# Kernel optimization log

Hardware: AMD Instinct MI355X
Metric: run time of the kernel (lower is better)

The kernel has to match this reference:

```python
import jax, jax.numpy as jnp
import numpy as np

BS, Q, S1, S2 = 8, 128, 32, 64
H_DIM, NH = 768, 12
DH = H_DIM // NH


def _linear_params(k, scale=0.02):
    kw, _ = jax.random.split(k)
    w = jax.random.normal(kw, (H_DIM, H_DIM), jnp.float32) * scale
    b = jnp.zeros((H_DIM,), jnp.float32)
    return w, b


def setup_inputs() -> dict:
    root = jax.random.key(0)
    ks = jax.random.split(root, 12)
    wq_w, wq_b = _linear_params(ks[0])
    wk_w, wk_b = _linear_params(ks[1])
    wv_w, wv_b = _linear_params(ks[2])
    sq_w, sq_b = _linear_params(ks[3])
    sk_w, sk_b = _linear_params(ks[4])
    sv_w, sv_b = _linear_params(ks[5])
    return {
        "q_in": jax.random.normal(ks[6], (BS, Q, H_DIM), jnp.float32),
        "k_in": jax.random.normal(ks[7], (BS, S1, S2, H_DIM), jnp.float32),
        "v_in": jax.random.normal(ks[8], (BS, S1, S2, H_DIM), jnp.float32),
        "kvec": jax.random.normal(ks[9], (BS, S1, H_DIM), jnp.float32),
        "word_mask": jnp.ones((BS, S1, S2), jnp.int32),
        "sentence_mask": jnp.ones((BS * Q, S1), jnp.int32),
        "wq_w": wq_w, "wq_b": wq_b, "wk_w": wk_w, "wk_b": wk_b,
        "wv_w": wv_w, "wv_b": wv_b, "sq_w": sq_w, "sq_b": sq_b,
        "sk_w": sk_w, "sk_b": sk_b, "sv_w": sv_w, "sv_b": sv_b,
    }


def reference(q_in, k_in, v_in, kvec, word_mask, sentence_mask,
              wq_w, wq_b, wk_w, wk_b, wv_w, wv_b,
              sq_w, sq_b, sk_w, sk_b, sv_w, sv_b):
    bs, q_len = q_in.shape[0], q_in.shape[1]
    s1, s2 = k_in.shape[1], k_in.shape[2]
    scale = 1.0 / jnp.sqrt(jnp.float32(DH))

    # additive masks, as in the torch module
    wm = (1.0 - word_mask.astype(jnp.float32)) * -10000.0      # [bs, s1, s2]
    sm = (1.0 - sentence_mask.astype(jnp.float32)) * -10000.0  # [bs*Q, s1]

    # ---- word-level attention ----
    q = (q_in @ wq_w + wq_b).reshape(bs, q_len, NH, DH)
    k = (k_in @ wk_w + wk_b).reshape(bs, s1, s2, NH, DH)
    v = (v_in @ wv_w + wv_b).reshape(bs, s1, s2, NH, DH)
    # scores over tokens within each sentence: [bs, s1, H, Q, s2]
    scores1 = jnp.einsum('bqhd,bsthd->bshqt', q, k) * scale
    probs1 = jax.nn.softmax(scores1 + wm[:, :, None, None, :], axis=-1)
    # word_hidden: [bs, Q, s1, h]
    wh = jnp.einsum('bshqt,bsthd->bqshd', probs1, v).reshape(bs, q_len, s1, H_DIM)

    # ---- sentence-level attention ----
    sq = (q_in @ sq_w + sq_b).reshape(bs, q_len, NH, DH)
    sk = (kvec @ sk_w + sk_b).reshape(bs, s1, NH, DH)   # shared across queries
    sv = (wh @ sv_w + sv_b).reshape(bs, q_len, s1, NH, DH)
    scores2 = jnp.einsum('bqhd,bshd->bqhs', sq, sk) * scale  # [bs, Q, H, s1]
    scores2 = scores2 + sm.reshape(bs, q_len, s1)[:, :, None, :]
    probs2 = jax.nn.softmax(scores2, axis=-1)
    out = jnp.einsum('bqhs,bqshd->bqhd', probs2, sv).reshape(bs * q_len, H_DIM)
    return out
```

## Files before the change

kernel.cpp:

```cpp
#include <hip/hip_runtime.h>
#include <hip/hip_bf16.h>


typedef __attribute__((ext_vector_type(8))) short short8;
typedef __attribute__((ext_vector_type(4))) short short4v;
typedef __attribute__((ext_vector_type(4))) float f32x4;

__device__ __forceinline__ short f2bf(float f) {
  __hip_bfloat16 b = __float2bfloat16(f);
  return __builtin_bit_cast(short, b);
}
__device__ __forceinline__ float bf2f(short s) {
  __hip_bfloat16 b = __builtin_bit_cast(__hip_bfloat16, s);
  return __bfloat162float(b);
}

#define MFMA16(a, b, c) __builtin_amdgcn_mfma_f32_16x16x32_bf16((a), (b), (c), 0, 0, 0)

__device__ __forceinline__ void async_load16(const short* g, short* l) {
  auto l3 = (__attribute__((address_space(3))) short*)(uintptr_t)(
      reinterpret_cast<uintptr_t>(l));
  auto g1 = (const __attribute__((address_space(1))) short*)g;
  __builtin_amdgcn_global_load_lds((const __attribute__((address_space(1))) void*)g1,
                                   (__attribute__((address_space(3))) void*)l3, 16, 0, 0);
}

__global__ __launch_bounds__(256)
void cvt_all(const float* __restrict__ q_in, const float* __restrict__ k_in,
             const float* __restrict__ v_in, const float* __restrict__ kvec,
             short* __restrict__ qbf, short* __restrict__ kbf,
             short* __restrict__ vbf, short* __restrict__ kvb) {
  const int i = blockIdx.x * 256 + threadIdx.x;
  const float* src;
  short* dst;
  int idx;
  if (i < 98304)        { src = q_in; dst = qbf; idx = i; }
  else if (i < 1671168) { src = k_in; dst = kbf; idx = i - 98304; }
  else if (i < 3244032) { src = v_in; dst = vbf; idx = i - 1671168; }
  else if (i < 3268608) { src = kvec; dst = kvb; idx = i - 3244032; }
  else return;
  const float4* s = (const float4*)src + (size_t)idx * 2;
  const float4 a = s[0], b = s[1];
  __align__(16) short tmp[8] = {f2bf(a.x), f2bf(a.y), f2bf(a.z), f2bf(a.w),
                                f2bf(b.x), f2bf(b.y), f2bf(b.z), f2bf(b.w)};
  *((short8*)dst + idx) = *(short8*)tmp;
}

__global__ __launch_bounds__(256)
void transpose_w6(const float* __restrict__ w0, const float* __restrict__ w1,
                  const float* __restrict__ w2, const float* __restrict__ w3,
                  const float* __restrict__ w4, const float* __restrict__ w5,
                  short* __restrict__ WT) {
  __shared__ float tile[32][33];
  const float* Ws[6] = {w0, w1, w2, w3, w4, w5};
  const float* W = Ws[blockIdx.z];
  short* WTo = WT + (size_t)blockIdx.z * 768 * 768;
  const int bx = blockIdx.x * 32, by = blockIdx.y * 32;
  const int tx = threadIdx.x, ty = threadIdx.y;
  #pragma unroll
  for (int i = 0; i < 32; i += 8)
    tile[ty + i][tx] = W[(size_t)(by + ty + i) * 768 + bx + tx];
  __syncthreads();
  #pragma unroll
  for (int i = 0; i < 32; i += 8)
    WTo[(size_t)(bx + ty + i) * 768 + by + tx] = f2bf(tile[tx][ty + i]);
}

template<int OUT_MODE>
__global__ __launch_bounds__(256)
void gemm_lds(const short* __restrict__ A, const short* __restrict__ WT,
              const float* __restrict__ bias, const float* __restrict__ bias2,
              const float* __restrict__ probs2, void* __restrict__ Outp,
              void* __restrict__ Outp2) {
  const int K = 768;
  __shared__ __align__(16) short As[128 * 32];
  __shared__ __align__(16) short Bs[128 * 32];
  const int tid = threadIdx.x;
  const int m0 = blockIdx.x * 128, n0 = blockIdx.y * 128;
  const int w = tid >> 6, lane = tid & 63, quad = lane >> 4, l16 = lane & 15;
  const int wm = (w >> 1) * 64, wn = (w & 1) * 64;

  const int grow = w * 32 + (lane >> 2);
  const int kc = (lane & 3) * 8;
  const short* ag = A + (size_t)(m0 + grow) * K + kc;
  const short* bg = WT + (size_t)(n0 + grow) * K + kc;
  short* al = &As[(w * 32) * 32];
  short* bl = &Bs[(w * 32) * 32];

  const f32x4 zero4 = {0.f, 0.f, 0.f, 0.f};
  f32x4 acc[4][4];
  #pragma unroll
  for (int i = 0; i < 4; i++)
    #pragma unroll
    for (int j = 0; j < 4; j++) acc[i][j] = zero4;

  for (int k0 = 0; k0 < K; k0 += 32) {
    __syncthreads();
    async_load16(ag, al);
    async_load16(ag + (size_t)16 * K, al + 16 * 32);
    async_load16(bg, bl);
    async_load16(bg + (size_t)16 * K, bl + 16 * 32);
    ag += 32;
    bg += 32;
    __syncthreads();
    short8 af[4], bf[4];
    #pragma unroll
    for (int i = 0; i < 4; i++)
      af[i] = *(short8*)&As[(wm + i * 16 + l16) * 32 + quad * 8];
    #pragma unroll
    for (int j = 0; j < 4; j++)
      bf[j] = *(short8*)&Bs[(wn + j * 16 + l16) * 32 + quad * 8];
    #pragma unroll
    for (int i = 0; i < 4; i++)
      #pragma unroll
      for (int j = 0; j < 4; j++)
        acc[i][j] = MFMA16(af[i], bf[j], acc[i][j]);
  }

  if (OUT_MODE == 4) {
    const int h = (n0 + wn) >> 6;
    const int bq0 = (m0 + wm) >> 5;
    float p2[2][2][4];
    #pragma unroll
    for (int g2 = 0; g2 < 2; g2++)
      #pragma unroll
      for (int par = 0; par < 2; par++)
        #pragma unroll
        for (int r = 0; r < 4; r++)
          p2[g2][par][r] =
              probs2[((size_t)(bq0 + g2) * 12 + h) * 32 + par * 16 + quad * 4 + r];
    float red[4][2];
    #pragma unroll
    for (int j = 0; j < 4; j++)
      #pragma unroll
      for (int g2 = 0; g2 < 2; g2++) {
        float ps = 0.f;
        #pragma unroll
        for (int par = 0; par < 2; par++)
          #pragma unroll
          for (int r = 0; r < 4; r++)
            ps += p2[g2][par][r] * acc[g2 * 2 + par][j][r];
        ps += __shfl_xor(ps, 16);
        ps += __shfl_xor(ps, 32);
        red[j][g2] = ps;
      }
    const int col = n0 + wn + quad * 16 + l16;
    const float bv = bias[col];
    float* outp = (float*)Outp;
    #pragma unroll
    for (int g2 = 0; g2 < 2; g2++)
      outp[(size_t)(bq0 + g2) * 768 + col] = red[quad][g2] + bv;
    return;
  }

  #pragma unroll
  for (int i = 0; i < 4; i++) {
    #pragma unroll
    for (int j = 0; j < 4; j++) {
      const int col = n0 + wn + j * 16 + l16;
      float bv;
      if (OUT_MODE == 3)
        bv = (col < 768) ? bias[col] : bias2[col - 768];
      else
        bv = bias[col];
      #pragma unroll
      for (int r = 0; r < 4; r++) {
        const int g = m0 + wm + i * 16 + quad * 4 + r;
        const float v = acc[i][j][r] + bv;
        if (OUT_MODE == 0) {
          ((float*)Outp)[(size_t)g * 768 + col] = v;
        } else {
          if (col < 768)
            ((short*)Outp)[(size_t)g * 768 + col] = f2bf(v);
          else
            ((float*)Outp2)[(size_t)g * 768 + (col - 768)] = v;
        }
      }
    }
  }
}

__global__ __launch_bounds__(256)
void gemm_kv(const short* __restrict__ kbf, const short* __restrict__ vbf,
             const short* __restrict__ WTk, const short* __restrict__ WTv,
             const float* __restrict__ kbias, const float* __restrict__ vbias,
             short* __restrict__ kp, short* __restrict__ vT) {
  const int K = 768;
  __shared__ __align__(16) short As[128 * 32];
  __shared__ __align__(16) short Bs[128 * 32];
  const int z = blockIdx.z;
  const short* A = z ? vbf : kbf;
  const short* WT = z ? WTv : WTk;
  const float* bias = z ? vbias : kbias;
  const int tid = threadIdx.x;
  const int m0 = blockIdx.x * 128, n0 = blockIdx.y * 128;
  const int w = tid >> 6, lane = tid & 63, quad = lane >> 4, l16 = lane & 15;
  const int wm = (w >> 1) * 64, wn = (w & 1) * 64;

  const int grow = w * 32 + (lane >> 2);
  const int kc = (lane & 3) * 8;
  const short* ag = A + (size_t)(m0 + grow) * K + kc;
  const short* bg = WT + (size_t)(n0 + grow) * K + kc;
  short* al = &As[(w * 32) * 32];
  short* bl = &Bs[(w * 32) * 32];

  const f32x4 zero4 = {0.f, 0.f, 0.f, 0.f};
  f32x4 acc[4][4];
  #pragma unroll
  for (int i = 0; i < 4; i++)
    #pragma unroll
    for (int j = 0; j < 4; j++) acc[i][j] = zero4;

  for (int k0 = 0; k0 < K; k0 += 32) {
    __syncthreads();
    async_load16(ag, al);
    async_load16(ag + (size_t)16 * K, al + 16 * 32);
    async_load16(bg, bl);
    async_load16(bg + (size_t)16 * K, bl + 16 * 32);
    ag += 32;
    bg += 32;
    __syncthreads();
    short8 af[4], bf[4];
    #pragma unroll
    for (int i = 0; i < 4; i++)
      af[i] = *(short8*)&As[(wm + i * 16 + l16) * 32 + quad * 8];
    #pragma unroll
    for (int j = 0; j < 4; j++)
      bf[j] = *(short8*)&Bs[(wn + j * 16 + l16) * 32 + quad * 8];
    #pragma unroll
    for (int i = 0; i < 4; i++)
      #pragma unroll
      for (int j = 0; j < 4; j++)
        acc[i][j] = MFMA16(af[i], bf[j], acc[i][j]);
  }

  if (z == 0) {
    #pragma unroll
    for (int i = 0; i < 4; i++)
      #pragma unroll
      for (int j = 0; j < 4; j++) {
        const int col = n0 + wn + j * 16 + l16;
        const float bv = bias[col];
        #pragma unroll
        for (int r = 0; r < 4; r++) {
          const int g = m0 + wm + i * 16 + quad * 4 + r;
          kp[(size_t)g * 768 + col] = f2bf(acc[i][j][r] + bv);
        }
      }
  } else {
    const int bs_ = (m0 + wm) >> 6;
    const int hh = (n0 + wn) >> 6;
    #pragma unroll
    for (int i = 0; i < 4; i++) {
      const int t0 = i * 16 + quad * 4;
      #pragma unroll
      for (int j = 0; j < 4; j++) {
        const int dd = j * 16 + l16;
        const float bv = bias[hh * 64 + dd];
        __align__(8) short tmp[4];
        #pragma unroll
        for (int r = 0; r < 4; r++) tmp[r] = f2bf(acc[i][j][r] + bv);
        *(short4v*)&vT[(((size_t)bs_ * 12 + hh) * 64 + dd) * 64 + t0] = *(short4v*)tmp;
      }
    }
  }
}

__global__ __launch_bounds__(256)
void word_attn(const short* __restrict__ q_proj, const short* __restrict__ k_proj,
               const short* __restrict__ vT, const int* __restrict__ word_mask,
               short* __restrict__ wh) {
  __shared__ __align__(16) short KVs[128 * 72];
  __shared__ __align__(16) short Ps[128 * 72];
  short* Ks = KVs;
  short* Vs = KVs + 64 * 72;
  short* Os = KVs;

  const int bid = blockIdx.x;
  const int h = bid % 12, s = (bid / 12) % 32, b = bid / (12 * 32);
  const int tid = threadIdx.x;
  const int w = tid >> 6, lane = tid & 63, quad = lane >> 4, l16 = lane & 15;
  const f32x4 zero4 = {0.f, 0.f, 0.f, 0.f};

  {
    const int t2 = tid & 127;
    const int row = t2 >> 1, half = (t2 & 1) * 32;
    const short* src;
    short* dst;
    if (tid < 128) {
      src = k_proj + ((size_t)((b * 32 + s) * 64 + row)) * 768 + h * 64 + half;
      dst = &Ks[row * 72 + half];
    } else {
      src = vT + ((size_t)((b * 32 + s) * 12 + h)) * 4096 + row * 64 + half;
      dst = &Vs[row * 72 + half];
    }
    #pragma unroll
    for (int i = 0; i < 4; i++)
      *(short8*)(dst + i * 8) = *(const short8*)(src + i * 8);
  }
  __syncthreads();

  f32x4 sac[2][4];
  #pragma unroll
  for (int i = 0; i < 2; i++)
    #pragma unroll
    for (int j = 0; j < 4; j++) sac[i][j] = zero4;
  {
    short8 aq[2][2], bk[4][2];
    #pragma unroll
    for (int i = 0; i < 2; i++)
      #pragma unroll
      for (int kb = 0; kb < 2; kb++)
        aq[i][kb] = *(const short8*)(q_proj +
            ((size_t)(b * 128 + w * 32 + i * 16 + l16)) * 768 + h * 64 + kb * 32 + quad * 8);
    #pragma unroll
    for (int j = 0; j < 4; j++)
      #pragma unroll
      for (int kb = 0; kb < 2; kb++)
        bk[j][kb] = *(short8*)&Ks[(j * 16 + l16) * 72 + kb * 32 + quad * 8];
    #pragma unroll
    for (int i = 0; i < 2; i++)
      #pragma unroll
      for (int j = 0; j < 4; j++) {
        sac[i][j] = MFMA16(aq[i][0], bk[j][0], sac[i][j]);
        sac[i][j] = MFMA16(aq[i][1], bk[j][1], sac[i][j]);
      }
  }

  {
    float wmv[4];
    const int* wmp = word_mask + (b * 32 + s) * 64;
    #pragma unroll
    for (int j = 0; j < 4; j++)
      wmv[j] = (1.0f - (float)wmp[j * 16 + l16]) * -10000.0f;
    #pragma unroll
    for (int i = 0; i < 2; i++) {
      #pragma unroll
      for (int r = 0; r < 4; r++) {
        float vv[4];
        float mx = -3.0e38f;
        #pragma unroll
        for (int j = 0; j < 4; j++) {
          const float val = sac[i][j][r] * 0.125f + wmv[j];
          vv[j] = val;
          mx = fmaxf(mx, val);
        }
        mx = fmaxf(mx, __shfl_xor(mx, 1));
        mx = fmaxf(mx, __shfl_xor(mx, 2));
        mx = fmaxf(mx, __shfl_xor(mx, 4));
        mx = fmaxf(mx, __shfl_xor(mx, 8));
        float sum = 0.f;
        #pragma unroll
        for (int j = 0; j < 4; j++) {
          vv[j] = __expf(vv[j] - mx);
          sum += vv[j];
        }
        sum += __shfl_xor(sum, 1);
        sum += __shfl_xor(sum, 2);
        sum += __shfl_xor(sum, 4);
        sum += __shfl_xor(sum, 8);
        const float inv = 1.0f / sum;
        const int row = w * 32 + i * 16 + quad * 4 + r;
        #pragma unroll
        for (int j = 0; j < 4; j++)
          Ps[row * 72 + j * 16 + l16] = f2bf(vv[j] * inv);
      }
    }
  }
  __syncthreads();

  f32x4 oac[2][4];
  #pragma unroll
  for (int i = 0; i < 2; i++)
    #pragma unroll
    for (int j = 0; j < 4; j++) oac[i][j] = zero4;
  {
    short8 ap[2][2], bv[4][2];
    #pragma unroll
    for (int i = 0; i < 2; i++)
      #pragma unroll
      for (int kb = 0; kb < 2; kb++)
        ap[i][kb] = *(short8*)&Ps[(w * 32 + i * 16 + l16) * 72 + kb * 32 + quad * 8];
    #pragma unroll
    for (int j = 0; j < 4; j++)
      #pragma unroll
      for (int kb = 0; kb < 2; kb++)
        bv[j][kb] = *(short8*)&Vs[(j * 16 + l16) * 72 + kb * 32 + quad * 8];
    #pragma unroll
    for (int i = 0; i < 2; i++)
      #pragma unroll
      for (int j = 0; j < 4; j++) {
        oac[i][j] = MFMA16(ap[i][0], bv[j][0], oac[i][j]);
        oac[i][j] = MFMA16(ap[i][1], bv[j][1], oac[i][j]);
      }
  }
  __syncthreads();
  #pragma unroll
  for (int i = 0; i < 2; i++)
    #pragma unroll
    for (int j = 0; j < 4; j++)
      #pragma unroll
      for (int r = 0; r < 4; r++)
        Os[(w * 32 + i * 16 + quad * 4 + r) * 72 + j * 16 + l16] = f2bf(oac[i][j][r]);
  __syncthreads();

  {
    const int row = tid >> 1, half = (tid & 1) * 32;
    short* dst = wh + (((size_t)(b * 128 + row)) * 32 + s) * 768 + h * 64 + half;
    const short* src = &Os[row * 72 + half];
    #pragma unroll
    for (int i = 0; i < 4; i++)
      *(short8*)(dst + i * 8) = *(const short8*)(src + i * 8);
  }
}

__global__ __launch_bounds__(256)
void sent_probs(const float* __restrict__ sq, const float* __restrict__ sk,
                const int* __restrict__ sent_mask, float* __restrict__ probs2) {
  __shared__ float sc[12 * 33];
  const int bid = blockIdx.x;
  const int b = bid >> 7, q = bid & 127;
  const int tid = threadIdx.x;

  for (int p = tid; p < 384; p += 256) {
    const int hh = p >> 5, ss = p & 31;
    const float4* a = (const float4*)(sq + ((size_t)(b * 128 + q)) * 768 + hh * 64);
    const float4* c = (const float4*)(sk + ((size_t)(b * 32 + ss)) * 768 + hh * 64);
    float d = 0.f;
    #pragma unroll
    for (int i = 0; i < 16; i++) {
      const float4 av = a[i], cv = c[i];
      d += av.x * cv.x + av.y * cv.y + av.z * cv.z + av.w * cv.w;
    }
    d = d * 0.125f + (1.0f - (float)sent_mask[(b * 128 + q) * 32 + ss]) * -10000.0f;
    sc[hh * 33 + ss] = d;
  }
  __syncthreads();
  if (tid < 12) {
    float mx = -3.0e38f;
    for (int ss = 0; ss < 32; ss++) mx = fmaxf(mx, sc[tid * 33 + ss]);
    float sum = 0.f;
    for (int ss = 0; ss < 32; ss++) {
      const float e = __expf(sc[tid * 33 + ss] - mx);
      sc[tid * 33 + ss] = e;
      sum += e;
    }
    const float inv = 1.0f / sum;
    for (int ss = 0; ss < 32; ss++) sc[tid * 33 + ss] *= inv;
  }
  __syncthreads();
  for (int p = tid; p < 384; p += 256) {
    const int hh = p >> 5, ss = p & 31;
    probs2[((size_t)bid * 12 + hh) * 32 + ss] = sc[hh * 33 + ss];
  }
}

extern "C" void kernel_launch(void* const* d_in, const int* in_sizes, int n_in,
                              void* d_out, int out_size, void* d_ws, size_t ws_size,
                              hipStream_t stream) {
  (void)in_sizes; (void)n_in; (void)out_size; (void)ws_size;
  const float* q_in      = (const float*)d_in[0];
  const float* k_in      = (const float*)d_in[1];
  const float* v_in      = (const float*)d_in[2];
  const float* kvec      = (const float*)d_in[3];
  const int*   word_mask = (const int*)d_in[4];
  const int*   sent_mask = (const int*)d_in[5];
  const float* wq_w = (const float*)d_in[6],  *wq_b = (const float*)d_in[7];
  const float* wk_w = (const float*)d_in[8],  *wk_b = (const float*)d_in[9];
  const float* wv_w = (const float*)d_in[10], *wv_b = (const float*)d_in[11];
  const float* sq_w = (const float*)d_in[12], *sq_b = (const float*)d_in[13];
  const float* sk_w = (const float*)d_in[14], *sk_b = (const float*)d_in[15];
  const float* sv_w = (const float*)d_in[16], *sv_b = (const float*)d_in[17];
  float* out = (float*)d_out;

  char* ws = (char*)d_ws;
  size_t off = 0;
  auto alloc = [&](size_t bytes) -> void* {
    void* p = ws + off;
    off += (bytes + 255) & ~(size_t)255;
    return p;
  };
  short* WT  = (short*)alloc((size_t)6 * 768 * 768 * 2);
  short* qbf = (short*)alloc((size_t)1024 * 768 * 2);
  short* kbf = (short*)alloc((size_t)16384 * 768 * 2);
  short* vbf = (short*)alloc((size_t)16384 * 768 * 2);
  short* kvb = (short*)alloc((size_t)256 * 768 * 2);
  short* qp  = (short*)alloc((size_t)1024 * 768 * 2);
  short* kp  = (short*)alloc((size_t)16384 * 768 * 2);
  short* vT  = (short*)alloc((size_t)16384 * 768 * 2);
  float* sqp = (float*)alloc((size_t)1024 * 768 * 4);
  float* skp = (float*)alloc((size_t)256 * 768 * 4);
  short* wh  = (short*)alloc((size_t)32768 * 768 * 2);
  float* pr2 = (float*)alloc((size_t)1024 * 12 * 32 * 4);

  const int WELEM = 768 * 768;

  transpose_w6<<<dim3(24, 24, 6), dim3(32, 8), 0, stream>>>(
      wq_w, sq_w, wk_w, wv_w, sk_w, sv_w, WT);
  cvt_all<<<dim3(12768), 256, 0, stream>>>(q_in, k_in, v_in, kvec, qbf, kbf, vbf, kvb);

  gemm_lds<3><<<dim3(8, 12), 256, 0, stream>>>(qbf, WT + 0 * WELEM, wq_b, sq_b,
                                               nullptr, qp, sqp);
  gemm_kv<<<dim3(128, 6, 2), 256, 0, stream>>>(kbf, vbf, WT + 2 * WELEM, WT + 3 * WELEM,
                                               wk_b, wv_b, kp, vT);
  gemm_lds<0><<<dim3(2, 6), 256, 0, stream>>>(kvb, WT + 4 * WELEM, sk_b, nullptr,
                                              nullptr, skp, nullptr);

  word_attn<<<dim3(3072), 256, 0, stream>>>(qp, kp, vT, word_mask, wh);

  sent_probs<<<dim3(1024), 256, 0, stream>>>(sqp, skp, sent_mask, pr2);

  gemm_lds<4><<<dim3(256, 6), 256, 0, stream>>>(wh, WT + 5 * WELEM, sv_b, nullptr,
                                                pr2, out, nullptr);
}
```

Before: 367.7 us.

## Fuse fp32-to-bf16 input conversion into projection GEMM loads with swizzled LDS

Removes the separate cvt_all pass over q/k/v/kvec. The projection GEMMs now load fp32 activations straight into LDS with async global-to-LDS copies and convert to bf16 while reading the MFMA fragments. This avoids writing and re-reading large bf16 copies of k_in and v_in. It also adds XOR swizzles to the A and B LDS layouts to reduce bank conflicts, and merges gemm_kv into a templated gemm. The cost is twice the LDS footprint and global traffic per A tile, plus conversion ALU work inside the inner loop.

```diff
diff --git a/kernel.cpp b/kernel.cpp
--- a/kernel.cpp
+++ b/kernel.cpp
@@ -17,33 +17,11 @@
 
 #define MFMA16(a, b, c) __builtin_amdgcn_mfma_f32_16x16x32_bf16((a), (b), (c), 0, 0, 0)
 
-__device__ __forceinline__ void async_load16(const short* g, short* l) {
-  auto l3 = (__attribute__((address_space(3))) short*)(uintptr_t)(
+__device__ __forceinline__ void async_load16(const void* g, void* l) {
+  auto l3 = (__attribute__((address_space(3))) void*)(uintptr_t)(
       reinterpret_cast<uintptr_t>(l));
-  auto g1 = (const __attribute__((address_space(1))) short*)g;
-  __builtin_amdgcn_global_load_lds((const __attribute__((address_space(1))) void*)g1,
-                                   (__attribute__((address_space(3))) void*)l3, 16, 0, 0);
-}
-
-__global__ __launch_bounds__(256)
-void cvt_all(const float* __restrict__ q_in, const float* __restrict__ k_in,
-             const float* __restrict__ v_in, const float* __restrict__ kvec,
-             short* __restrict__ qbf, short* __restrict__ kbf,
-             short* __restrict__ vbf, short* __restrict__ kvb) {
-  const int i = blockIdx.x * 256 + threadIdx.x;
-  const float* src;
-  short* dst;
-  int idx;
-  if (i < 98304)        { src = q_in; dst = qbf; idx = i; }
-  else if (i < 1671168) { src = k_in; dst = kbf; idx = i - 98304; }
-  else if (i < 3244032) { src = v_in; dst = vbf; idx = i - 1671168; }
-  else if (i < 3268608) { src = kvec; dst = kvb; idx = i - 3244032; }
-  else return;
-  const float4* s = (const float4*)src + (size_t)idx * 2;
-  const float4 a = s[0], b = s[1];
-  __align__(16) short tmp[8] = {f2bf(a.x), f2bf(a.y), f2bf(a.z), f2bf(a.w),
-                                f2bf(b.x), f2bf(b.y), f2bf(b.z), f2bf(b.w)};
-  *((short8*)dst + idx) = *(short8*)tmp;
+  auto g1 = (const __attribute__((address_space(1))) void*)g;
+  __builtin_amdgcn_global_load_lds(g1, l3, 16, 0, 0);
 }
 
 __global__ __launch_bounds__(256)
@@ -66,26 +44,41 @@
     WTo[(size_t)(bx + ty + i) * 768 + by + tx] = f2bf(tile[tx][ty + i]);
 }
 
-template<int OUT_MODE>
+template<int A_FP32, int OUT_MODE>
 __global__ __launch_bounds__(256)
-void gemm_lds(const short* __restrict__ A, const short* __restrict__ WT,
-              const float* __restrict__ bias, const float* __restrict__ bias2,
-              const float* __restrict__ probs2, void* __restrict__ Outp,
-              void* __restrict__ Outp2) {
-  const int K = 768;
-  __shared__ __align__(16) short As[128 * 32];
+void gemm(const void* __restrict__ Ap, const void* __restrict__ Ap2,
+          const short* __restrict__ WTa, const short* __restrict__ WTb,
+          const float* __restrict__ bias_a, const float* __restrict__ bias_b,
+          const float* __restrict__ probs2, void* __restrict__ Outp,
+          void* __restrict__ Outp2) {
+  __shared__ __align__(16) short As[A_FP32 ? 128 * 64 : 128 * 32];
   __shared__ __align__(16) short Bs[128 * 32];
+  float* Alf = (float*)As;
+
+  const int z = (OUT_MODE == 5) ? blockIdx.z : 0;
+  const void* A = (OUT_MODE == 5 && z) ? Ap2 : Ap;
+  const short* WT = (OUT_MODE == 5 && z) ? WTb : WTa;
+  const float* bias = (OUT_MODE == 5 && z) ? bias_b : bias_a;
+
   const int tid = threadIdx.x;
   const int m0 = blockIdx.x * 128, n0 = blockIdx.y * 128;
   const int w = tid >> 6, lane = tid & 63, quad = lane >> 4, l16 = lane & 15;
   const int wm = (w >> 1) * 64, wn = (w & 1) * 64;
 
-  const int grow = w * 32 + (lane >> 2);
-  const int kc = (lane & 3) * 8;
-  const short* ag = A + (size_t)(m0 + grow) * K + kc;
-  const short* bg = WT + (size_t)(n0 + grow) * K + kc;
-  short* al = &As[(w * 32) * 32];
+  const int brow = lane >> 2, bpos = lane & 3;
+  const int bsw = bpos ^ ((brow >> 1) & 3);
+  const short* bg = WT + (size_t)(n0 + w * 32 + brow) * 768 + bsw * 8;
   short* bl = &Bs[(w * 32) * 32];
+
+  const float* agf = nullptr;
+  const short* agb = nullptr;
+  if (A_FP32) {
+    const int arow = lane >> 3, apos = lane & 7;
+    const int asw = apos ^ arow;
+    agf = (const float*)A + (size_t)(m0 + w * 32 + arow) * 768 + asw * 4;
+  } else {
+    agb = (const short*)A + (size_t)(m0 + w * 32 + brow) * 768 + bsw * 8;
+  }
 
   const f32x4 zero4 = {0.f, 0.f, 0.f, 0.f};
   f32x4 acc[4][4];
@@ -94,22 +87,47 @@
     #pragma unroll
     for (int j = 0; j < 4; j++) acc[i][j] = zero4;
 
-  for (int k0 = 0; k0 < K; k0 += 32) {
+  for (int k0 = 0; k0 < 768; k0 += 32) {
     __syncthreads();
-    async_load16(ag, al);
-    async_load16(ag + (size_t)16 * K, al + 16 * 32);
-    async_load16(bg, bl);
-    async_load16(bg + (size_t)16 * K, bl + 16 * 32);
-    ag += 32;
-    bg += 32;
+    if (A_FP32) {
+      const float* s = agf + k0;
+      float* d = Alf + (w * 32) * 32;
+      async_load16(s, d);
+      async_load16(s + (size_t)8 * 768, d + 8 * 32);
+      async_load16(s + (size_t)16 * 768, d + 16 * 32);
+      async_load16(s + (size_t)24 * 768, d + 24 * 32);
+    } else {
+      const short* s = agb + k0;
+      short* d = &As[(w * 32) * 32];
+      async_load16(s, d);
+      async_load16(s + (size_t)16 * 768, d + 16 * 32);
+    }
+    {
+      const short* s = bg + k0;
+      async_load16(s, bl);
+      async_load16(s + (size_t)16 * 768, bl + 16 * 32);
+    }
     __syncthreads();
+
     short8 af[4], bf[4];
     #pragma unroll
-    for (int i = 0; i < 4; i++)
-      af[i] = *(short8*)&As[(wm + i * 16 + l16) * 32 + quad * 8];
-    #pragma unroll
-    for (int j = 0; j < 4; j++)
-      bf[j] = *(short8*)&Bs[(wn + j * 16 + l16) * 32 + quad * 8];
+    for (int i = 0; i < 4; i++) {
+      const int row = wm + i * 16 + l16;
+      if (A_FP32) {
+        const f32x4 lo = *(const f32x4*)&Alf[row * 32 + (((quad * 2) ^ (row & 7)) * 4)];
+        const f32x4 hi = *(const f32x4*)&Alf[row * 32 + (((quad * 2 + 1) ^ (row & 7)) * 4)];
+        __align__(16) short t[8] = {f2bf(lo.x), f2bf(lo.y), f2bf(lo.z), f2bf(lo.w),
+                                    f2bf(hi.x), f2bf(hi.y), f2bf(hi.z), f2bf(hi.w)};
+        af[i] = *(short8*)t;
+      } else {
+        af[i] = *(short8*)&As[row * 32 + ((quad ^ ((row >> 1) & 3)) * 8)];
+      }
+    }
+    #pragma unroll
+    for (int j = 0; j < 4; j++) {
+      const int row = wn + j * 16 + l16;
+      bf[j] = *(short8*)&Bs[row * 32 + ((quad ^ ((row >> 1) & 3)) * 8)];
+    }
     #pragma unroll
     for (int i = 0; i < 4; i++)
       #pragma unroll
@@ -153,6 +171,26 @@
     return;
   }
 
+  if (OUT_MODE == 5 && z == 1) {
+    const int bs_ = (m0 + wm) >> 6;
+    const int hh = (n0 + wn) >> 6;
+    short* vT = (short*)Outp2;
+    #pragma unroll
+    for (int i = 0; i < 4; i++) {
+      const int t0 = i * 16 + quad * 4;
+      #pragma unroll
+      for (int j = 0; j < 4; j++) {
+        const int dd = j * 16 + l16;
+        const float bv = bias[hh * 64 + dd];
+        __align__(8) short tmp[4];
+        #pragma unroll
+        for (int r = 0; r < 4; r++) tmp[r] = f2bf(acc[i][j][r] + bv);
+        *(short4v*)&vT[(((size_t)bs_ * 12 + hh) * 64 + dd) * 64 + t0] = *(short4v*)tmp;
+      }
+    }
+    return;
+  }
+
   #pragma unroll
   for (int i = 0; i < 4; i++) {
     #pragma unroll
@@ -160,7 +198,7 @@
       const int col = n0 + wn + j * 16 + l16;
       float bv;
       if (OUT_MODE == 3)
-        bv = (col < 768) ? bias[col] : bias2[col - 768];
+        bv = (col < 768) ? bias_a[col] : bias_b[col - 768];
       else
         bv = bias[col];
       #pragma unroll
@@ -169,98 +207,14 @@
         const float v = acc[i][j][r] + bv;
         if (OUT_MODE == 0) {
           ((float*)Outp)[(size_t)g * 768 + col] = v;
+        } else if (OUT_MODE == 5) {
+          ((short*)Outp)[(size_t)g * 768 + col] = f2bf(v);
         } else {
           if (col < 768)
             ((short*)Outp)[(size_t)g * 768 + col] = f2bf(v);
           else
             ((float*)Outp2)[(size_t)g * 768 + (col - 768)] = v;
         }
-      }
-    }
-  }
-}
-
-__global__ __launch_bounds__(256)
-void gemm_kv(const short* __restrict__ kbf, const short* __restrict__ vbf,
-             const short* __restrict__ WTk, const short* __restrict__ WTv,
-             const float* __restrict__ kbias, const float* __restrict__ vbias,
-             short* __restrict__ kp, short* __restrict__ vT) {
-  const int K = 768;
-  __shared__ __align__(16) short As[128 * 32];
-  __shared__ __align__(16) short Bs[128 * 32];
-  const int z = blockIdx.z;
-  const short* A = z ? vbf : kbf;
-  const short* WT = z ? WTv : WTk;
-  const float* bias = z ? vbias : kbias;
-  const int tid = threadIdx.x;
-  const int m0 = blockIdx.x * 128, n0 = blockIdx.y * 128;
-  const int w = tid >> 6, lane = tid & 63, quad = lane >> 4, l16 = lane & 15;
-  const int wm = (w >> 1) * 64, wn = (w & 1) * 64;
-
-  const int grow = w * 32 + (lane >> 2);
-  const int kc = (lane & 3) * 8;
-  const short* ag = A + (size_t)(m0 + grow) * K + kc;
-  const short* bg = WT + (size_t)(n0 + grow) * K + kc;
-  short* al = &As[(w * 32) * 32];
-  short* bl = &Bs[(w * 32) * 32];
-
-  const f32x4 zero4 = {0.f, 0.f, 0.f, 0.f};
-  f32x4 acc[4][4];
-  #pragma unroll
-  for (int i = 0; i < 4; i++)
-    #pragma unroll
-    for (int j = 0; j < 4; j++) acc[i][j] = zero4;
-
-  for (int k0 = 0; k0 < K; k0 += 32) {
-    __syncthreads();
-    async_load16(ag, al);
-    async_load16(ag + (size_t)16 * K, al + 16 * 32);
-    async_load16(bg, bl);
-    async_load16(bg + (size_t)16 * K, bl + 16 * 32);
-    ag += 32;
-    bg += 32;
-    __syncthreads();
-    short8 af[4], bf[4];
-    #pragma unroll
-    for (int i = 0; i < 4; i++)
-      af[i] = *(short8*)&As[(wm + i * 16 + l16) * 32 + quad * 8];
-    #pragma unroll
-    for (int j = 0; j < 4; j++)
-      bf[j] = *(short8*)&Bs[(wn + j * 16 + l16) * 32 + quad * 8];
-    #pragma unroll
-    for (int i = 0; i < 4; i++)
-      #pragma unroll
-      for (int j = 0; j < 4; j++)
-        acc[i][j] = MFMA16(af[i], bf[j], acc[i][j]);
-  }
-
-  if (z == 0) {
-    #pragma unroll
-    for (int i = 0; i < 4; i++)
-      #pragma unroll
-      for (int j = 0; j < 4; j++) {
-        const int col = n0 + wn + j * 16 + l16;
-        const float bv = bias[col];
-        #pragma unroll
-        for (int r = 0; r < 4; r++) {
-          const int g = m0 + wm + i * 16 + quad * 4 + r;
-          kp[(size_t)g * 768 + col] = f2bf(acc[i][j][r] + bv);
-        }
-      }
-  } else {
-    const int bs_ = (m0 + wm) >> 6;
-    const int hh = (n0 + wn) >> 6;
-    #pragma unroll
-    for (int i = 0; i < 4; i++) {
-      const int t0 = i * 16 + quad * 4;
-      #pragma unroll
-      for (int j = 0; j < 4; j++) {
-        const int dd = j * 16 + l16;
-        const float bv = bias[hh * 64 + dd];
-        __align__(8) short tmp[4];
-        #pragma unroll
-        for (int r = 0; r < 4; r++) tmp[r] = f2bf(acc[i][j][r] + bv);
-        *(short4v*)&vT[(((size_t)bs_ * 12 + hh) * 64 + dd) * 64 + t0] = *(short4v*)tmp;
       }
     }
   }
@@ -481,10 +435,6 @@
     return p;
   };
   short* WT  = (short*)alloc((size_t)6 * 768 * 768 * 2);
-  short* qbf = (short*)alloc((size_t)1024 * 768 * 2);
-  short* kbf = (short*)alloc((size_t)16384 * 768 * 2);
-  short* vbf = (short*)alloc((size_t)16384 * 768 * 2);
-  short* kvb = (short*)alloc((size_t)256 * 768 * 2);
   short* qp  = (short*)alloc((size_t)1024 * 768 * 2);
   short* kp  = (short*)alloc((size_t)16384 * 768 * 2);
   short* vT  = (short*)alloc((size_t)16384 * 768 * 2);
@@ -497,19 +447,18 @@
 
   transpose_w6<<<dim3(24, 24, 6), dim3(32, 8), 0, stream>>>(
       wq_w, sq_w, wk_w, wv_w, sk_w, sv_w, WT);
-  cvt_all<<<dim3(12768), 256, 0, stream>>>(q_in, k_in, v_in, kvec, qbf, kbf, vbf, kvb);
-
-  gemm_lds<3><<<dim3(8, 12), 256, 0, stream>>>(qbf, WT + 0 * WELEM, wq_b, sq_b,
-                                               nullptr, qp, sqp);
-  gemm_kv<<<dim3(128, 6, 2), 256, 0, stream>>>(kbf, vbf, WT + 2 * WELEM, WT + 3 * WELEM,
-                                               wk_b, wv_b, kp, vT);
-  gemm_lds<0><<<dim3(2, 6), 256, 0, stream>>>(kvb, WT + 4 * WELEM, sk_b, nullptr,
-                                              nullptr, skp, nullptr);
+
+  gemm<1, 3><<<dim3(8, 12), 256, 0, stream>>>(
+      q_in, nullptr, WT + 0 * WELEM, nullptr, wq_b, sq_b, nullptr, qp, sqp);
+  gemm<1, 5><<<dim3(128, 6, 2), 256, 0, stream>>>(
+      k_in, v_in, WT + 2 * WELEM, WT + 3 * WELEM, wk_b, wv_b, nullptr, kp, vT);
+  gemm<1, 0><<<dim3(2, 6), 256, 0, stream>>>(
+      kvec, nullptr, WT + 4 * WELEM, nullptr, sk_b, nullptr, nullptr, skp, nullptr);
 
   word_attn<<<dim3(3072), 256, 0, stream>>>(qp, kp, vT, word_mask, wh);
 
   sent_probs<<<dim3(1024), 256, 0, stream>>>(sqp, skp, sent_mask, pr2);
 
-  gemm_lds<4><<<dim3(256, 6), 256, 0, stream>>>(wh, WT + 5 * WELEM, sv_b, nullptr,
-                                                pr2, out, nullptr);
-}
+  gemm<0, 4><<<dim3(256, 6), 256, 0, stream>>>(
+      wh, nullptr, WT + 5 * WELEM, nullptr, sv_b, nullptr, pr2, out, nullptr);
+}
```

New measurement: 382.8 us. 4.1% more time.
